# Kernel tuning notes

Measured on AMD Instinct MI355X. Metric: run time of the kernel, lower is better.

## Reference

```python
import jax, jax.numpy as jnp
import numpy as np

N_HEADS = 16
ROPE_BASE = 10000.0


def apply_rope(x):
    # x: (b, h, t, d); rotate interleaved pairs along last dim, positions = t axis
    b, h, t, d = x.shape
    theta = 1.0 / (ROPE_BASE ** (jnp.arange(0, d, 2, dtype=jnp.float32) / d))  # (d/2,)
    ang = jnp.arange(t, dtype=jnp.float32)[:, None] * theta[None, :]           # (t, d/2)
    cos = jnp.cos(ang)[None, None]  # (1,1,t,d/2)
    sin = jnp.sin(ang)[None, None]
    xp = x.reshape(b, h, t, d // 2, 2)
    x0, x1 = xp[..., 0], xp[..., 1]
    o0 = x0 * cos - x1 * sin
    o1 = x1 * cos + x0 * sin
    return jnp.stack([o0, o1], axis=-1).reshape(b, h, t, d)


def setup_inputs() -> dict:
    key = jax.random.key(0)
    k1, k2, k3 = jax.random.split(key, 3)
    B, T, C = 2, 2048, 1024
    x = jax.random.normal(k1, (B, T, C), dtype=jnp.float32)
    w_qkv = jax.random.normal(k2, (3 * C, C), dtype=jnp.float32) * (1.0 / np.sqrt(C))
    w_proj = jax.random.normal(k3, (C, C), dtype=jnp.float32) * (1.0 / np.sqrt(C))
    return {"x": x, "w_qkv": w_qkv, "w_proj": w_proj}


def reference(x, w_qkv, w_proj):
    B, T, C = x.shape
    H = N_HEADS
    D = C // H
    # fused QKV projection: (b,t,3C)
    qkv = x @ w_qkv.T
    qkv = qkv.reshape(B, T, 3, H, D).transpose(2, 0, 3, 1, 4)  # (3, b, h, t, d)
    q, k, v = qkv[0], qkv[1], qkv[2]
    q = apply_rope(q)
    k = apply_rope(k)
    scale = 1.0 / jnp.sqrt(jnp.float32(D))
    scores = jnp.einsum('bhqd,bhkd->bhqk', q, k) * scale  # (b,h,t,t)
    causal = jnp.tril(jnp.ones((T, T), dtype=bool))
    scores = jnp.where(causal[None, None], scores, jnp.finfo(scores.dtype).min)
    attn = jax.nn.softmax(scores, axis=-1)
    y = jnp.einsum('bhqk,bhkd->bhqd', attn, v)  # (b,h,t,d)
    y = y.transpose(0, 2, 1, 3).reshape(B, T, C)
    return y @ w_proj.T
```

## Files before the change

kernel.cpp:

```cpp
#include <hip/hip_runtime.h>
#include <math.h>

#define B_ 2
#define T_ 2048
#define C_ 1024
#define H_ 16
#define D_ 64
#define NX_ 4194304
#define NWQ_ 3145728
#define NWP_ 1048576

typedef unsigned short u16;
typedef unsigned int u32;
typedef __bf16 bf16x8 __attribute__((ext_vector_type(8)));
typedef _Float16 f16x8 __attribute__((ext_vector_type(8)));
typedef __fp16 fp16x2 __attribute__((ext_vector_type(2)));
typedef float f32x4 __attribute__((ext_vector_type(4)));
typedef u16 u16x4 __attribute__((ext_vector_type(4)));

__device__ __forceinline__ u16 f2bf(float f) {
    union { float f; u32 u; } v; v.f = f;
    u32 r = v.u + 0x7fffu + ((v.u >> 16) & 1u);
    return (u16)(r >> 16);
}

#define GLD_LDS(g, l) \
    __builtin_amdgcn_global_load_lds( \
        (const __attribute__((address_space(1))) u32*)(const void*)(g), \
        (__attribute__((address_space(3))) u32*)(void*)(l), 16, 0, 0)

__global__ __launch_bounds__(256) void cast_all(const float* __restrict__ x,
                                                const float* __restrict__ wq,
                                                const float* __restrict__ wp,
                                                u16* __restrict__ out) {
    const int i = (blockIdx.x * 256 + threadIdx.x) * 4;
    const float* src;
    int off;
    if (i < NX_) { src = x; off = i; }
    else if (i < NX_ + NWQ_) { src = wq; off = i - NX_; }
    else { src = wp; off = i - NX_ - NWQ_; }
    float4 v = *(const float4*)(src + off);
    u16x4 o;
    o.x = f2bf(v.x); o.y = f2bf(v.y); o.z = f2bf(v.z); o.w = f2bf(v.w);
    *(u16x4*)(out + i) = o;
}

template <int EPI>
__global__ __launch_bounds__(256) void gemm64(const u16* __restrict__ A,
                                              const u16* __restrict__ Bm,
                                              float* __restrict__ OutF,
                                              u16* __restrict__ qb,
                                              u16* __restrict__ kb,
                                              u16* __restrict__ vt,
                                              int M, int N, int K) {
    __shared__ u16 As[128 * 64];
    __shared__ u16 Bs[128 * 64];
    const int tid = threadIdx.x;
    const int lane = tid & 63;
    const int wave = tid >> 6;
    const int wm = (wave >> 1) * 64;
    const int wn = (wave & 1) * 64;
    const int m0 = blockIdx.y * 128;
    const int n0 = blockIdx.x * 128;

    const int rl = lane >> 3;
    const int sg = ((lane & 7) ^ rl) * 8;
    const u16* gA[4]; const u16* gB[4];
    u16 *lA[4], *lB[4];
    #pragma unroll
    for (int c = 0; c < 4; ++c) {
        const int ca = wave * 4 + c;
        gA[c] = A + (size_t)(m0 + ca * 8 + rl) * K + sg;
        gB[c] = Bm + (size_t)(n0 + ca * 8 + rl) * K + sg;
        lA[c] = As + ca * 512;
        lB[c] = Bs + ca * 512;
    }

    const int col = lane & 15;
    const int quad = lane >> 4;
    int aoff[2][4], boff[2][4];
    #pragma unroll
    for (int ks = 0; ks < 2; ++ks)
        #pragma unroll
        for (int i = 0; i < 4; ++i) {
            const int m = wm + i * 16 + col;
            aoff[ks][i] = (m >> 3) * 512 + (m & 7) * 64 +
                          ((((ks << 2) | quad)) ^ (m & 7)) * 8;
            const int n = wn + i * 16 + col;
            boff[ks][i] = (n >> 3) * 512 + (n & 7) * 64 +
                          ((((ks << 2) | quad)) ^ (n & 7)) * 8;
        }

    f32x4 acc[4][4] = {};
    for (int k0 = 0; k0 < K; k0 += 64) {
        __syncthreads();
        #pragma unroll
        for (int c = 0; c < 4; ++c) {
            GLD_LDS(gA[c] + k0, lA[c]);
            GLD_LDS(gB[c] + k0, lB[c]);
        }
        __syncthreads();
        #pragma unroll
        for (int ks = 0; ks < 2; ++ks) {
            bf16x8 a[4], b[4];
            #pragma unroll
            for (int i = 0; i < 4; ++i) a[i] = *(const bf16x8*)(As + aoff[ks][i]);
            #pragma unroll
            for (int j = 0; j < 4; ++j) b[j] = *(const bf16x8*)(Bs + boff[ks][j]);
            #pragma unroll
            for (int i = 0; i < 4; ++i)
                #pragma unroll
                for (int j = 0; j < 4; ++j)
                    acc[i][j] = __builtin_amdgcn_mfma_f32_16x16x32_bf16(
                        a[i], b[j], acc[i][j], 0, 0, 0);
        }
    }

    const int rq = quad * 4;
    if (EPI == 0) {
        #pragma unroll
        for (int i = 0; i < 4; ++i)
            #pragma unroll
            for (int j = 0; j < 4; ++j)
                #pragma unroll
                for (int r = 0; r < 4; ++r)
                    OutF[(size_t)(m0 + wm + i * 16 + rq + r) * N +
                         n0 + wn + j * 16 + col] = acc[i][j][r];
    } else {
        const int sslot = m0 >> 10;
        #pragma unroll
        for (int i = 0; i < 4; ++i) {
            const int gm = m0 + wm + i * 16 + rq;
            const int hh = (gm >> 6) & 15;
            const int dbase = gm & 63;
            #pragma unroll
            for (int j = 0; j < 4; ++j) {
                const int gt = n0 + wn + j * 16 + col;
                const int bb = gt >> 11;
                const int t = gt & (T_ - 1);
                const int bh = bb * H_ + hh;
                if (sslot < 2) {
                    const float tf = (float)t;
                    u16x4 ov;
                    #pragma unroll
                    for (int p = 0; p < 2; ++p) {
                        const float ip = (float)((dbase >> 1) + p);
                        const float theta = __expf(-0.2878231366f * ip);
                        const float ang = tf * theta;
                        float sn, cs; __sincosf(ang, &sn, &cs);
                        const float x0 = acc[i][j][2 * p];
                        const float x1 = acc[i][j][2 * p + 1];
                        ov[2 * p]     = f2bf(x0 * cs - x1 * sn);
                        ov[2 * p + 1] = f2bf(x1 * cs + x0 * sn);
                    }
                    u16* dst = (sslot == 0 ? qb : kb) +
                               ((size_t)bh * T_ + t) * D_ + dbase;
                    *(u16x4*)dst = ov;
                } else {
                    #pragma unroll
                    for (int r = 0; r < 4; ++r) {
                        union { _Float16 h; u16 u; } cv;
                        cv.h = (_Float16)acc[i][j][r];
                        vt[((size_t)bh * D_ + dbase + r) * T_ + t] = cv.u;
                    }
                }
            }
        }
    }
}

__global__ __launch_bounds__(256) void attn_mfma(const u16* __restrict__ qb,
                                                 const u16* __restrict__ kb,
                                                 const u16* __restrict__ vtg,
                                                 u16* __restrict__ y) {
    __shared__ u16 Ks[8 * 512];
    __shared__ u16 Vt[8 * 512];
    __shared__ u16 Ps[4][32 * 72];
    const int b = blockIdx.z, h = blockIdx.y;
    const int bh = b * H_ + h;
    const int qt = gridDim.x - 1 - blockIdx.x;
    const int q0 = qt * 128;
    const int tid = threadIdx.x;
    const int lane = tid & 63;
    const int wave = tid >> 6;
    const int col = lane & 15;
    const int quad = lane >> 4;

    const u16* qbase = qb + ((size_t)bh * T_ + q0 + wave * 32) * D_;
    bf16x8 qf[2][2];
    #pragma unroll
    for (int qh = 0; qh < 2; ++qh)
        #pragma unroll
        for (int ks = 0; ks < 2; ++ks)
            qf[qh][ks] = *(const bf16x8*)(qbase + (qh * 16 + col) * D_ +
                                          ks * 32 + quad * 8);

    f32x4 o[2][4] = {};
    float lsum[2] = {0.0f, 0.0f};

    const int rl = lane >> 3;
    const int sg = ((lane & 7) ^ rl) * 8;
    const u16* kg[2]; const u16* vg[2];
    u16 *lk[2], *lv[2];
    #pragma unroll
    for (int e = 0; e < 2; ++e) {
        const int ca = 2 * wave + e;
        kg[e] = kb + ((size_t)bh * T_ + ca * 8 + rl) * D_ + sg;
        vg[e] = vtg + ((size_t)bh * D_ + ca * 8 + rl) * T_ + sg;
        lk[e] = Ks + ca * 512;
        lv[e] = Vt + ca * 512;
    }
    u16* Pw = &Ps[wave][0];

    int koff[2][4];
    #pragma unroll
    for (int ks = 0; ks < 2; ++ks)
        #pragma unroll
        for (int n = 0; n < 4; ++n) {
            const int rr = n * 16 + col;
            koff[ks][n] = (rr >> 3) * 512 + (rr & 7) * 64 +
                          ((((ks << 2) | quad)) ^ (rr & 7)) * 8;
        }

    const int nchunks = 2 * qt + 2;
    for (int ci = 0; ci < nchunks; ++ci) {
        const int j0 = ci * 64;
        __syncthreads();
        #pragma unroll
        for (int e = 0; e < 2; ++e) {
            GLD_LDS(kg[e] + (size_t)j0 * D_, lk[e]);
            GLD_LDS(vg[e] + j0, lv[e]);
        }
        __syncthreads();

        f32x4 s[2][4] = {};
        #pragma unroll
        for (int ks = 0; ks < 2; ++ks) {
            #pragma unroll
            for (int n = 0; n < 4; ++n) {
                const bf16x8 kf = *(const bf16x8*)(Ks + koff[ks][n]);
                #pragma unroll
                for (int qh = 0; qh < 2; ++qh)
                    s[qh][n] = __builtin_amdgcn_mfma_f32_16x16x32_bf16(
                        kf, qf[qh][ks], s[qh][n], 0, 0, 0);
            }
        }

        const bool diag = (ci >= nchunks - 2);
        #pragma unroll
        for (int qh = 0; qh < 2; ++qh) {
            const int qrow = q0 + wave * 32 + qh * 16 + col;
            #pragma unroll
            for (int n = 0; n < 4; ++n) {
                float p[4];
                #pragma unroll
                for (int r = 0; r < 4; ++r) {
                    const float xv = s[qh][n][r] * 0.1803368801f;
                    float pv = __builtin_amdgcn_exp2f(fminf(xv, 80.0f));
                    if (diag && (j0 + n * 16 + quad * 4 + r > qrow)) pv = 0.0f;
                    p[r] = pv;
                    lsum[qh] += pv;
                }
                union { fp16x2 h[2]; u32 u[2]; } pk;
                pk.h[0] = __builtin_amdgcn_cvt_pkrtz(p[0], p[1]);
                pk.h[1] = __builtin_amdgcn_cvt_pkrtz(p[2], p[3]);
                *(uint2*)(Pw + (qh * 16 + col) * 72 + n * 16 + quad * 4) =
                    make_uint2(pk.u[0], pk.u[1]);
            }
        }

        #pragma unroll
        for (int ks = 0; ks < 2; ++ks) {
            f16x8 pf[2];
            #pragma unroll
            for (int qh = 0; qh < 2; ++qh)
                pf[qh] = *(const f16x8*)(Pw + (qh * 16 + col) * 72 +
                                         ks * 32 + quad * 8);
            #pragma unroll
            for (int n = 0; n < 4; ++n) {
                const f16x8 vf = *(const f16x8*)(Vt + koff[ks][n]);
                #pragma unroll
                for (int qh = 0; qh < 2; ++qh)
                    o[qh][n] = __builtin_amdgcn_mfma_f32_16x16x32_f16(
                        pf[qh], vf, o[qh][n], 0, 0, 0);
            }
        }
    }

    #pragma unroll
    for (int qh = 0; qh < 2; ++qh) {
        float l = lsum[qh];
        l += __shfl_xor(l, 16);
        l += __shfl_xor(l, 32);
        const float inv = 1.0f / l;
        float invr[4];
        #pragma unroll
        for (int r = 0; r < 4; ++r)
            invr[r] = __shfl(inv, quad * 4 + r);
        #pragma unroll
        for (int r = 0; r < 4; ++r) {
            const int row = q0 + wave * 32 + qh * 16 + quad * 4 + r;
            u16* yp = y + (size_t)(b * T_ + row) * C_ + h * D_;
            #pragma unroll
            for (int n = 0; n < 4; ++n)
                yp[n * 16 + col] = f2bf(o[qh][n][r] * invr[r]);
        }
    }
}

extern "C" void kernel_launch(void* const* d_in, const int* in_sizes, int n_in,
                              void* d_out, int out_size, void* d_ws, size_t ws_size,
                              hipStream_t stream) {
    const float* x      = (const float*)d_in[0];
    const float* w_qkv  = (const float*)d_in[1];
    const float* w_proj = (const float*)d_in[2];
    float* out = (float*)d_out;

    const int M = B_ * T_;
    u16* xb  = (u16*)d_ws;
    u16* wqb = xb + NX_;
    u16* wpb = wqb + NWQ_;
    u16* qb  = wpb + NWP_;
    u16* kb  = qb + NX_;
    u16* vt  = kb + NX_;
    u16* yb  = vt + NX_;

    cast_all<<<(NX_ + NWQ_ + NWP_) / 1024, 256, 0, stream>>>(x, w_qkv, w_proj, xb);

    gemm64<1><<<dim3(M / 128, 3 * C_ / 128), 256, 0, stream>>>(
        wqb, xb, nullptr, qb, kb, vt, 3 * C_, M, C_);

    attn_mfma<<<dim3(T_ / 128, H_, B_), 256, 0, stream>>>(qb, kb, vt, yb);

    gemm64<0><<<dim3(C_ / 128, M / 128), 256, 0, stream>>>(
        yb, wpb, out, nullptr, nullptr, nullptr, M, C_, C_);
}
```

Before: 206.8 us.

## Double-buffer K/V tiles in attention and remap grid for causal load balance

The attention kernel now keeps two shared-memory buffers for K and V. It issues the async global-to-LDS loads for the next 64-key chunk before computing on the current one, which removes the second barrier per iteration and overlaps memory with the MFMA work. The 3D grid becomes a flat 512-block grid that schedules the heavy (late) query tiles first and the light ones after, to balance the causal workload across CUs. The cost is double the K/V shared memory, which may reduce occupancy, and the correctness of the overlap depends on the barrier draining the outstanding loads.

Measured after the change: 190.0 us. 8.1% less time.

```diff
diff --git a/kernel.cpp b/kernel.cpp
--- a/kernel.cpp
+++ b/kernel.cpp
@@ -173,12 +173,13 @@
                                                  const u16* __restrict__ kb,
                                                  const u16* __restrict__ vtg,
                                                  u16* __restrict__ y) {
-    __shared__ u16 Ks[8 * 512];
-    __shared__ u16 Vt[8 * 512];
+    __shared__ u16 Ks[2][8 * 512];
+    __shared__ u16 Vt[2][8 * 512];
     __shared__ u16 Ps[4][32 * 72];
-    const int b = blockIdx.z, h = blockIdx.y;
-    const int bh = b * H_ + h;
-    const int qt = gridDim.x - 1 - blockIdx.x;
+    const int id = blockIdx.x;
+    const int qt = (id < 256) ? (15 - (id >> 5)) : ((id - 256) >> 5);
+    const int bh = id & 31;
+    const int b = bh >> 4, h = bh & 15;
     const int q0 = qt * 128;
     const int tid = threadIdx.x;
     const int lane = tid & 63;
@@ -201,14 +202,13 @@
     const int rl = lane >> 3;
     const int sg = ((lane & 7) ^ rl) * 8;
     const u16* kg[2]; const u16* vg[2];
-    u16 *lk[2], *lv[2];
+    int lco[2];
     #pragma unroll
     for (int e = 0; e < 2; ++e) {
         const int ca = 2 * wave + e;
         kg[e] = kb + ((size_t)bh * T_ + ca * 8 + rl) * D_ + sg;
         vg[e] = vtg + ((size_t)bh * D_ + ca * 8 + rl) * T_ + sg;
-        lk[e] = Ks + ca * 512;
-        lv[e] = Vt + ca * 512;
+        lco[e] = ca * 512;
     }
     u16* Pw = &Ps[wave][0];
 
@@ -223,22 +223,31 @@
         }
 
     const int nchunks = 2 * qt + 2;
+    #pragma unroll
+    for (int e = 0; e < 2; ++e) {
+        GLD_LDS(kg[e], &Ks[0][lco[e]]);
+        GLD_LDS(vg[e], &Vt[0][lco[e]]);
+    }
+
     for (int ci = 0; ci < nchunks; ++ci) {
+        const int buf = ci & 1;
         const int j0 = ci * 64;
         __syncthreads();
-        #pragma unroll
-        for (int e = 0; e < 2; ++e) {
-            GLD_LDS(kg[e] + (size_t)j0 * D_, lk[e]);
-            GLD_LDS(vg[e] + j0, lv[e]);
-        }
-        __syncthreads();
+        if (ci + 1 < nchunks) {
+            const size_t j1 = (size_t)(ci + 1) * 64;
+            #pragma unroll
+            for (int e = 0; e < 2; ++e) {
+                GLD_LDS(kg[e] + j1 * D_, &Ks[buf ^ 1][lco[e]]);
+                GLD_LDS(vg[e] + j1, &Vt[buf ^ 1][lco[e]]);
+            }
+        }
 
         f32x4 s[2][4] = {};
         #pragma unroll
         for (int ks = 0; ks < 2; ++ks) {
             #pragma unroll
             for (int n = 0; n < 4; ++n) {
-                const bf16x8 kf = *(const bf16x8*)(Ks + koff[ks][n]);
+                const bf16x8 kf = *(const bf16x8*)(&Ks[buf][koff[ks][n]]);
                 #pragma unroll
                 for (int qh = 0; qh < 2; ++qh)
                     s[qh][n] = __builtin_amdgcn_mfma_f32_16x16x32_bf16(
@@ -278,7 +287,7 @@
                                          ks * 32 + quad * 8);
             #pragma unroll
             for (int n = 0; n < 4; ++n) {
-                const f16x8 vf = *(const f16x8*)(Vt + koff[ks][n]);
+                const f16x8 vf = *(const f16x8*)(&Vt[buf][koff[ks][n]]);
                 #pragma unroll
                 for (int qh = 0; qh < 2; ++qh)
                     o[qh][n] = __builtin_amdgcn_mfma_f32_16x16x32_f16(
@@ -330,7 +339,7 @@
     gemm64<1><<<dim3(M / 128, 3 * C_ / 128), 256, 0, stream>>>(
         wqb, xb, nullptr, qb, kb, vt, 3 * C_, M, C_);
 
-    attn_mfma<<<dim3(T_ / 128, H_, B_), 256, 0, stream>>>(qb, kb, vt, yb);
+    attn_mfma<<<512, 256, 0, stream>>>(qb, kb, vt, yb);
 
     gemm64<0><<<dim3(C_ / 128, M / 128), 256, 0, stream>>>(
         yb, wpb, out, nullptr, nullptr, nullptr, M, C_, C_);
```
